# Performance work log

Measured on AMD Instinct MI355X. Metric: run time of the kernel, lower is better.

The kernel has to match this reference:

```python
import jax, jax.numpy as jnp
import numpy as np

B, P, G, C = 64, 5000, 300, 20   # images, preds/img, gt/img, num classes
INPUT_SIZE = 512.0
IOU_THRESH = 0.5


def setup_inputs() -> dict:
    key = jax.random.key(0)
    k1, k2, k3, k4, k5, k6, k7 = jax.random.split(key, 7)
    # predictions: [x1,y1,x2,y2,score,cls], boxes normalized to [0,1]
    pxy = jax.random.uniform(k1, (B, P, 2), minval=0.0, maxval=0.8)
    pwh = jax.random.uniform(k2, (B, P, 2), minval=0.02, maxval=0.2)
    score = jax.random.uniform(k3, (B, P, 1))
    pcls = jax.random.randint(k4, (B, P, 1), 0, C).astype(jnp.float32)
    output = jnp.concatenate([pxy, pxy + pwh, score, pcls], axis=-1)
    # ground truth: [x1,y1,x2,y2,cls]
    txy = jax.random.uniform(k5, (B, G, 2), minval=0.0, maxval=0.8)
    twh = jax.random.uniform(k6, (B, G, 2), minval=0.02, maxval=0.2)
    tcls = jax.random.randint(k7, (B, G, 1), 0, C).astype(jnp.float32)
    labels = jnp.concatenate([txy, txy + twh, tcls], axis=-1)
    return {"output": output, "labels": labels}


def reference(output, labels):
    scale = jnp.array([INPUT_SIZE, INPUT_SIZE, INPUT_SIZE, INPUT_SIZE], dtype=output.dtype)

    def match_image(preds, targets):  # preds [P,6], targets [G,5]
        tcls = targets[:, 4]
        tboxes = targets[:, :4] * scale                     # [G,4]
        tarea = (tboxes[:, 2] - tboxes[:, 0]) * (tboxes[:, 3] - tboxes[:, 1])

        def step(detected, pred):
            pbox = pred[:4] * scale
            lt = jnp.maximum(pbox[:2], tboxes[:, :2])       # [G,2]
            rb = jnp.minimum(pbox[2:], tboxes[:, 2:])
            wh = jnp.clip(rb - lt, 0.0)
            inter = wh[:, 0] * wh[:, 1]
            parea = (pbox[2] - pbox[0]) * (pbox[3] - pbox[1])
            ious = inter / (parea + tarea - inter)          # [G]
            cls_mask = tcls == pred[5]
            masked = jnp.where(cls_mask, ious, -1.0)
            bi = jnp.argmax(masked)                          # greedy argmax over same-class gt
            match = ((pred[4] > 0)
                     & jnp.any(cls_mask)
                     & (masked[bi] > IOU_THRESH)
                     & (~detected[bi]))                      # sequential dedup
            detected = detected.at[bi].set(detected[bi] | match)
            return detected, match

        _, correct = jax.lax.scan(step, jnp.zeros(tboxes.shape[0], dtype=bool), preds)
        return correct                                       # [P] bool

    correct = jax.vmap(match_image)(output, labels).astype(output.dtype)  # [B,P]
    # stats: (correct flag, score, predicted class) per prediction; tcls per image
    stats = jnp.stack([correct, output[:, :, 4], output[:, :, 5]], axis=-1)  # [B,P,3]
    tcls = labels[:, :, 4]                                                    # [B,G]
    return stats, tcls
```

## Files before the change

kernel.cpp:

```cpp
#include <hip/hip_runtime.h>
#include <cstdint>

#define B 64
#define P 5000
#define G 300
#define C 20
#define SCALE_F 512.0f
#define IOU_TH 0.5f
#define NT 1024
#define PPT ((P + NT - 1) / NT)

#pragma clang fp contract(off)

__global__ __launch_bounds__(NT) void fused_kernel(
    const float* __restrict__ preds,
    const float* __restrict__ labels,
    float* __restrict__ out_stats,
    float* __restrict__ out_tcls)
{
    const int b = blockIdx.x;
    const int tid = threadIdx.x;

    __shared__ float4 sb[G];
    __shared__ float  sa[G];
    __shared__ short  ssi[G];
    __shared__ short  cls_s[G];
    __shared__ int    so[C + 1];
    __shared__ int    cnt[C];
    __shared__ int    firstp[G];
    __shared__ int    poff[C + 1];
    __shared__ int    pcnt[C];
    __shared__ unsigned short psorted[P];
    __shared__ short  pbi[P];

    const float* lab = labels + (size_t)b * G * 5;
    const float* prd = preds + (size_t)b * P * 6;

    if (tid < C) { cnt[tid] = 0; pcnt[tid] = 0; }
    for (int t = tid; t < G; t += NT) {
        float c = lab[t * 5 + 4];
        cls_s[t] = (short)(int)c;
        out_tcls[b * G + t] = c;
        firstp[t] = 0x7FFFFFFF;
    }
    __syncthreads();

    for (int t = tid; t < G; t += NT) atomicAdd(&cnt[cls_s[t]], 1);
    #pragma unroll
    for (int k = 0; k < PPT; ++k) {
        int p = tid + k * NT;
        if (p < P) {
            float score = prd[p * 6 + 4];
            float fcls  = prd[p * 6 + 5];
            atomicAdd(&pcnt[(int)fcls], 1);
            size_t op = (size_t)b * P + p;
            out_stats[op * 3 + 1] = score;
            out_stats[op * 3 + 2] = fcls;
        }
    }
    __syncthreads();

    if (tid == 0) {
        int a = 0;
        for (int c = 0; c < C; ++c) { so[c] = a; a += cnt[c]; }
        so[C] = a;
    }
    if (tid == 64) {
        int a = 0;
        for (int c = 0; c < C; ++c) { int v = pcnt[c]; poff[c] = a; pcnt[c] = a; a += v; }
        poff[C] = a;
    }
    __syncthreads();

    for (int t = tid; t < G; t += NT) {
        short c = cls_s[t];
        int rank = 0;
        for (int u = 0; u < t; ++u) rank += (cls_s[u] == c) ? 1 : 0;
        int pos = so[c] + rank;
        float x1 = lab[t * 5 + 0] * SCALE_F;
        float y1 = lab[t * 5 + 1] * SCALE_F;
        float x2 = lab[t * 5 + 2] * SCALE_F;
        float y2 = lab[t * 5 + 3] * SCALE_F;
        sb[pos] = make_float4(x1, y1, x2, y2);
        sa[pos] = (x2 - x1) * (y2 - y1);
        ssi[pos] = (short)t;
    }
    #pragma unroll
    for (int k = 0; k < PPT; ++k) {
        int p = tid + k * NT;
        if (p < P) {
            int c = (int)prd[p * 6 + 5];
            int pos = atomicAdd(&pcnt[c], 1);
            psorted[pos] = (unsigned short)p;
        }
    }
    __syncthreads();

    #pragma unroll
    for (int k = 0; k < PPT; ++k) {
        int slot = tid + k * NT;
        if (slot >= P) continue;
        int p = psorted[slot];
        const float* pr = prd + p * 6;
        float px1 = pr[0] * SCALE_F;
        float py1 = pr[1] * SCALE_F;
        float px2 = pr[2] * SCALE_F;
        float py2 = pr[3] * SCALE_F;
        float score = pr[4];
        int c = (int)pr[5];
        float parea = (px2 - px1) * (py2 - py1);

        int lo = so[c], hi = so[c + 1];
        float best = -1.0f;
        int bi = -1;
        for (int j = lo; j < hi; ++j) {
            float4 tb = sb[j];
            float lx = fmaxf(px1, tb.x);
            float ly = fmaxf(py1, tb.y);
            float rx = fminf(px2, tb.z);
            float ry = fminf(py2, tb.w);
            float w = fmaxf(rx - lx, 0.0f);
            float h = fmaxf(ry - ly, 0.0f);
            float inter = w * h;
            float uni = (parea + sa[j]) - inter;
            float iou = inter / uni;
            if (iou > best) { best = iou; bi = ssi[j]; }
        }

        bool eligible = (score > 0.0f) && (hi > lo) && (best > IOU_TH);
        pbi[p] = eligible ? (short)bi : (short)-1;
        if (eligible) atomicMin(&firstp[bi], p);
    }
    __syncthreads();

    #pragma unroll
    for (int k = 0; k < PPT; ++k) {
        int p = tid + k * NT;
        if (p >= P) continue;
        int bi = pbi[p];
        float corr = (bi >= 0 && firstp[bi] == p) ? 1.0f : 0.0f;
        out_stats[((size_t)b * P + p) * 3 + 0] = corr;
    }
}

extern "C" void kernel_launch(void* const* d_in, const int* in_sizes, int n_in,
                              void* d_out, int out_size, void* d_ws, size_t ws_size,
                              hipStream_t stream) {
    const float* output = (const float*)d_in[0];
    const float* labels = (const float*)d_in[1];

    float* out_stats = (float*)d_out;
    float* out_tcls  = (float*)d_out + (size_t)B * P * 3;

    fused_kernel<<<B, NT, 0, stream>>>(output, labels, out_stats, out_tcls);
}
```

Before: 84.13 us.

## Split per-image matching across multiple blocks with global atomic dedup and resolve pass

Work for each image is now spread over four blocks of 512 threads, giving 256 blocks instead of 64 so more of the GPU's compute units are busy. Deduplication of matched ground-truth boxes moves from shared-memory atomicMin to global atomicMin on a workspace buffer, and a memset is issued first to initialise it. A second kernel then decides which prediction owns each ground-truth box. The cost is two extra launches (memset and resolve), global atomics, and the label setup being repeated in every chunk block.

```diff
diff --git a/kernel.cpp b/kernel.cpp
--- a/kernel.cpp
+++ b/kernel.cpp
@@ -7,18 +7,23 @@
 #define C 20
 #define SCALE_F 512.0f
 #define IOU_TH 0.5f
-#define NT 1024
-#define PPT ((P + NT - 1) / NT)
+#define NSPLIT 4
+#define PCHUNK ((P + NSPLIT - 1) / NSPLIT)
+#define NTA 512
+#define SPT ((PCHUNK + NTA - 1) / NTA)
 
 #pragma clang fp contract(off)
 
-__global__ __launch_bounds__(NT) void fused_kernel(
+__global__ __launch_bounds__(NTA) void match_kernel(
     const float* __restrict__ preds,
     const float* __restrict__ labels,
     float* __restrict__ out_stats,
-    float* __restrict__ out_tcls)
+    float* __restrict__ out_tcls,
+    unsigned int* __restrict__ gfirstp,
+    short* __restrict__ gbest)
 {
-    const int b = blockIdx.x;
+    const int s = blockIdx.x;
+    const int b = blockIdx.y;
     const int tid = threadIdx.x;
 
     __shared__ float4 sb[G];
@@ -27,29 +32,26 @@
     __shared__ short  cls_s[G];
     __shared__ int    so[C + 1];
     __shared__ int    cnt[C];
-    __shared__ int    firstp[G];
-    __shared__ int    poff[C + 1];
     __shared__ int    pcnt[C];
-    __shared__ unsigned short psorted[P];
-    __shared__ short  pbi[P];
+    __shared__ unsigned short psorted[PCHUNK];
 
     const float* lab = labels + (size_t)b * G * 5;
     const float* prd = preds + (size_t)b * P * 6;
+    const int pbase = s * PCHUNK;
 
     if (tid < C) { cnt[tid] = 0; pcnt[tid] = 0; }
-    for (int t = tid; t < G; t += NT) {
+    for (int t = tid; t < G; t += NTA) {
         float c = lab[t * 5 + 4];
         cls_s[t] = (short)(int)c;
-        out_tcls[b * G + t] = c;
-        firstp[t] = 0x7FFFFFFF;
+        if (s == 0) out_tcls[b * G + t] = c;
     }
     __syncthreads();
 
-    for (int t = tid; t < G; t += NT) atomicAdd(&cnt[cls_s[t]], 1);
+    for (int t = tid; t < G; t += NTA) atomicAdd(&cnt[cls_s[t]], 1);
     #pragma unroll
-    for (int k = 0; k < PPT; ++k) {
-        int p = tid + k * NT;
-        if (p < P) {
+    for (int k = 0; k < SPT; ++k) {
+        int p = pbase + k * NTA + tid;
+        if (p < pbase + PCHUNK && p < P) {
             float score = prd[p * 6 + 4];
             float fcls  = prd[p * 6 + 5];
             atomicAdd(&pcnt[(int)fcls], 1);
@@ -67,12 +69,11 @@
     }
     if (tid == 64) {
         int a = 0;
-        for (int c = 0; c < C; ++c) { int v = pcnt[c]; poff[c] = a; pcnt[c] = a; a += v; }
-        poff[C] = a;
+        for (int c = 0; c < C; ++c) { int v = pcnt[c]; pcnt[c] = a; a += v; }
     }
     __syncthreads();
 
-    for (int t = tid; t < G; t += NT) {
+    for (int t = tid; t < G; t += NTA) {
         short c = cls_s[t];
         int rank = 0;
         for (int u = 0; u < t; ++u) rank += (cls_s[u] == c) ? 1 : 0;
@@ -86,9 +87,9 @@
         ssi[pos] = (short)t;
     }
     #pragma unroll
-    for (int k = 0; k < PPT; ++k) {
-        int p = tid + k * NT;
-        if (p < P) {
+    for (int k = 0; k < SPT; ++k) {
+        int p = pbase + k * NTA + tid;
+        if (p < pbase + PCHUNK && p < P) {
             int c = (int)prd[p * 6 + 5];
             int pos = atomicAdd(&pcnt[c], 1);
             psorted[pos] = (unsigned short)p;
@@ -97,9 +98,9 @@
     __syncthreads();
 
     #pragma unroll
-    for (int k = 0; k < PPT; ++k) {
-        int slot = tid + k * NT;
-        if (slot >= P) continue;
+    for (int k = 0; k < SPT; ++k) {
+        int slot = k * NTA + tid;
+        if (slot >= PCHUNK) continue;
         int p = psorted[slot];
         const float* pr = prd + p * 6;
         float px1 = pr[0] * SCALE_F;
@@ -128,19 +129,23 @@
         }
 
         bool eligible = (score > 0.0f) && (hi > lo) && (best > IOU_TH);
-        pbi[p] = eligible ? (short)bi : (short)-1;
-        if (eligible) atomicMin(&firstp[bi], p);
+        gbest[(size_t)b * P + p] = eligible ? (short)bi : (short)-1;
+        if (eligible) atomicMin(&gfirstp[b * G + bi], (unsigned int)p);
     }
-    __syncthreads();
+}
 
-    #pragma unroll
-    for (int k = 0; k < PPT; ++k) {
-        int p = tid + k * NT;
-        if (p >= P) continue;
-        int bi = pbi[p];
-        float corr = (bi >= 0 && firstp[bi] == p) ? 1.0f : 0.0f;
-        out_stats[((size_t)b * P + p) * 3 + 0] = corr;
-    }
+__global__ __launch_bounds__(256) void resolve_kernel(
+    const unsigned int* __restrict__ gfirstp,
+    const short* __restrict__ gbest,
+    float* __restrict__ out_stats)
+{
+    int i = blockIdx.x * 256 + threadIdx.x;
+    if (i >= B * P) return;
+    int b = i / P;
+    int p = i - b * P;
+    int bi = gbest[i];
+    float corr = (bi >= 0 && gfirstp[b * G + bi] == (unsigned int)p) ? 1.0f : 0.0f;
+    out_stats[(size_t)i * 3 + 0] = corr;
 }
 
 extern "C" void kernel_launch(void* const* d_in, const int* in_sizes, int n_in,
@@ -152,5 +157,13 @@
     float* out_stats = (float*)d_out;
     float* out_tcls  = (float*)d_out + (size_t)B * P * 3;
 
-    fused_kernel<<<B, NT, 0, stream>>>(output, labels, out_stats, out_tcls);
+    unsigned int* gfirstp = (unsigned int*)d_ws;
+    short* gbest          = (short*)(gfirstp + B * G);
+
+    hipMemsetAsync(gfirstp, 0xFF, (size_t)B * G * 4, stream);
+
+    dim3 grid(NSPLIT, B);
+    match_kernel<<<grid, NTA, 0, stream>>>(output, labels, out_stats, out_tcls,
+                                           gfirstp, gbest);
+    resolve_kernel<<<(B * P + 255) / 256, 256, 0, stream>>>(gfirstp, gbest, out_stats);
 }
```

Result: faster. 77.30 us (-8.1%).
